# Performance work log

Hardware: AMD Instinct MI355X
Metric: run time of the kernel (lower is better)

## Reference

```python
import jax, jax.numpy as jnp
import numpy as np

BS, N = 8, 2000
ALPHA = 0.2  # LeakyReLU slope
NEG = -9e15


def _gat_head(x, adj, W, a):
    # x: [bs,N,Fin], W: [Fin,Fout], a: [2*Fout]
    h = x @ W                                   # [bs,N,F]
    F_ = W.shape[-1]
    # e_ij = lrelu(h_i . a[:F] + h_j . a[F:])  (decomposed form of concat+matmul)
    src = h @ a[:F_]                            # [bs,N]
    dst = h @ a[F_:]                            # [bs,N]
    e = jax.nn.leaky_relu(src[:, :, None] + dst[:, None, :], ALPHA)  # [bs,N,N]
    att = jnp.where(adj[None] > 0, e, NEG)
    att = jax.nn.softmax(att, axis=-1)
    return jax.nn.elu(att @ h)                  # [bs,N,F]


def _gat_multihead(x, adj, W, a):
    # W: [H,Fin,Fout], a: [H,2*Fout] -> concat heads on feature dim
    out = jax.vmap(_gat_head, in_axes=(None, None, 0, 0))(x, adj, W, a)  # [H,bs,N,F]
    H, bs, n, F_ = out.shape
    return jnp.moveaxis(out, 0, 2).reshape(bs, n, H * F_)


def setup_inputs() -> dict:
    key = jax.random.key(0)
    ks = jax.random.split(key, 20)
    g = 1.414

    def xavu(k, shape, gain=1.0):
        fan_in, fan_out = shape[-2], shape[-1]
        lim = gain * np.sqrt(6.0 / (fan_in + fan_out))
        return jax.random.uniform(k, shape, jnp.float32, -lim, lim)

    x = jax.random.normal(ks[0], (BS, N, 1), jnp.float32)
    adj = jax.random.randint(ks[1], (N, N), 0, 2).astype(jnp.float32)
    inp = {
        "x": x, "adj": adj,
        "W1": xavu(ks[2], (4, 1, 8), g), "a1": xavu(ks[3], (4, 16, 1), g)[..., 0],
        "W2": xavu(ks[4], (3, 32, 16), g), "a2": xavu(ks[5], (3, 32, 1), g)[..., 0],
        "pw1": xavu(ks[6], (32, 1))[:, 0], "pb1": jnp.zeros((1,), jnp.float32),
        "pw2": xavu(ks[7], (48, 1))[:, 0], "pb2": jnp.zeros((1,), jnp.float32),
        "fc1_w": xavu(ks[8], (3 * N, 600)), "fc1_b": jnp.zeros((600,), jnp.float32),
        "fc2_w": xavu(ks[9], (600, 256)), "fc2_b": jnp.zeros((256,), jnp.float32),
        "fc3_w": xavu(ks[10], (256, 64)), "fc3_b": jnp.zeros((64,), jnp.float32),
        "fc4_w": xavu(ks[11], (64, 32)), "fc4_b": jnp.zeros((32,), jnp.float32),
        "fc5_w": xavu(ks[12], (32, 2)), "fc5_b": jnp.zeros((2,), jnp.float32),
    }
    return inp


def reference(x, adj, W1, a1, W2, a2, pw1, pb1, pw2, pb2,
              fc1_w, fc1_b, fc2_w, fc2_b, fc3_w, fc3_b, fc4_w, fc4_b, fc5_w, fc5_b):
    # dropout layers are identity in eval mode
    x0 = jnp.mean(x, axis=-1)                       # [bs,N]
    h = _gat_multihead(x, adj, W1, a1)              # [bs,N,32]
    x1 = h @ pw1 + pb1                              # [bs,N]
    h = _gat_multihead(h, adj, W2, a2)              # [bs,N,48]
    x2 = h @ pw2 + pb2                              # [bs,N]
    z = jnp.concatenate([x0, x1, x2], axis=1)       # [bs,3N]
    z = jax.nn.elu(z @ fc1_w + fc1_b)
    z = jax.nn.elu(z @ fc2_w + fc2_b)
    z1 = jax.nn.elu(z @ fc3_w + fc3_b)              # output [bs,64]
    z = jax.nn.elu(z1 @ fc4_w + fc4_b)
    gat_out = z @ fc5_w + fc5_b                     # [bs,2]
    return (z1, gat_out)
```

## Files before the change

kernel.cpp:

```cpp
#include <hip/hip_runtime.h>
#include <hip/hip_bf16.h>
#include <cmath>

#define N_NODES 2000
#define BS 8

typedef __attribute__((ext_vector_type(8))) short short8v;
typedef __attribute__((ext_vector_type(4))) float float4v;

__device__ __forceinline__ float elu_f(float v) { return v > 0.f ? v : expm1f(v); }

__device__ __forceinline__ unsigned short f32_bf16u(float f) {
    __hip_bfloat16 h = __float2bfloat16(f);
    unsigned short u;
    __builtin_memcpy(&u, &h, 2);
    return u;
}
__device__ __forceinline__ short f32_bf16(float f) { return (short)f32_bf16u(f); }

__device__ __forceinline__ unsigned cvt_pk_bf16(float lo, float hi) {
    unsigned r;
    asm("v_cvt_pk_bf16_f32 %0, %1, %2" : "=v"(r) : "v"(lo), "v"(hi));
    return r;
}

__global__ __launch_bounds__(256) void pack_kernel(
    const float* __restrict__ adj, const float* __restrict__ x,
    const float* __restrict__ W1, const float* __restrict__ a1,
    unsigned* __restrict__ maskT32, short* __restrict__ hT,
    short* __restrict__ xb16,
    float* __restrict__ PQ1, float* __restrict__ md1) {
    __shared__ float2 redmm[256];
    int bx = blockIdx.x;
    int tid = threadIdx.x;
    if (bx < N_NODES) {
        int row = bx;
        int lane = tid & 63, wv = tid >> 6;
        for (int wq = wv; wq < 32; wq += 4) {
            int j = wq * 64 + lane;
            bool on = (j < N_NODES) && (adj[(size_t)row * N_NODES + j] > 0.f);
            unsigned long long bal = __ballot(on);
            if (lane == 0) {
                maskT32[(size_t)(2 * wq) * 2048 + row] = (unsigned)bal;
                maskT32[(size_t)(2 * wq + 1) * 2048 + row] = (unsigned)(bal >> 32);
            }
        }
        return;
    }
    if (bx == N_NODES) {
        for (int i = tid; i < 24 * 16 * 48; i += 256) {
            int bh = i / 768, rem = i % 768, f = rem / 48, n = N_NODES + rem % 48;
            hT[((size_t)bh * 16 + f) * 2048 + n] = 0;
        }
        return;
    }
    if (bx == N_NODES + 1) {
        for (int i = tid; i < BS * 2048; i += 256) {
            int b = i >> 11, n = i & 2047;
            xb16[i] = (n < N_NODES) ? f32_bf16(x[(size_t)b * N_NODES + n]) : 0;
        }
        return;
    }
    int bh = bx - (N_NODES + 2);
    int b = bh >> 2, h = bh & 3;
    float ws = 0.f, wd = 0.f;
    #pragma unroll
    for (int f = 0; f < 8; ++f) {
        float wv = W1[h * 8 + f];
        ws = fmaf(wv, a1[h * 16 + f], ws);
        wd = fmaf(wv, a1[h * 16 + 8 + f], wd);
    }
    float mn = 1e30f, mx = -1e30f;
    for (int n = tid; n < N_NODES; n += 256) {
        float v = x[(size_t)b * N_NODES + n];
        mn = fminf(mn, v); mx = fmaxf(mx, v);
    }
    redmm[tid] = make_float2(mn, mx);
    __syncthreads();
    for (int s = 128; s > 0; s >>= 1) {
        if (tid < s) {
            redmm[tid].x = fminf(redmm[tid].x, redmm[tid + s].x);
            redmm[tid].y = fmaxf(redmm[tid].y, redmm[tid + s].y);
        }
        __syncthreads();
    }
    float md = wd >= 0.f ? wd * redmm[0].y : wd * redmm[0].x;
    if (tid == 0) md1[bh] = md;
    float2* pq = (float2*)PQ1 + (size_t)bh * 2048;
    for (int n = tid; n < 2048; n += 256) {
        if (n < N_NODES) {
            float d = wd * x[(size_t)b * N_NODES + n] - md;
            pq[n] = make_float2(__expf(d), __expf(0.2f * d));
        } else {
            pq[n] = make_float2(0.f, 0.f);
        }
    }
}

__global__ __launch_bounds__(256) void att1_kernel(
    const unsigned* __restrict__ maskT32,
    const float* __restrict__ x, const short* __restrict__ xb16,
    const float* __restrict__ PQ1, const float* __restrict__ md1,
    const float* __restrict__ W1, const float* __restrict__ a1,
    float* __restrict__ pn1, float* __restrict__ pd1) {
    __shared__ float2 sPQ[1024];
    int tid = threadIdx.x;
    int head = blockIdx.y;
    int half = blockIdx.z & 1, b = blockIdx.z >> 1;
    int bh = b * 4 + head;
    int j0g = half * 1024;

    const float2* pq = (const float2*)PQ1 + (size_t)bh * 2048 + j0g;
    for (int i = tid; i < 1024; i += 256) sPQ[i] = pq[i];

    float ws = 0.f;
    #pragma unroll
    for (int f = 0; f < 8; ++f)
        ws = fmaf(W1[head * 8 + f], a1[head * 16 + f], ws);
    float md = md1[bh];
    __syncthreads();

    int lane = tid & 63;
    int wave = __builtin_amdgcn_readfirstlane(tid >> 6);
    int t = blockIdx.x * 4 + wave;
    if (t >= 125) return;
    int rs = lane & 15;
    int g = lane >> 4;
    int row = t * 16 + rs;

    float xr = x[(size_t)b * N_NODES + row];
    float u = ws * xr + md;
    float c = __expf(-0.8f * u);

    unsigned fill = (rs == 1) ? 0x3F803F80u : 0u;
    bool isx = (rs == 0);
    const short* xbp = xb16 + (size_t)b * 2048 + j0g;

    float4v acc = {0.f, 0.f, 0.f, 0.f};

    for (int jcl = 0; jcl < 32; ++jcl) {
        int jb = jcl * 32 + g * 8;
        float4 pqa0 = *(const float4*)(&sPQ[jb]);
        float4 pqa1 = *(const float4*)(&sPQ[jb + 2]);
        float4 pqa2 = *(const float4*)(&sPQ[jb + 4]);
        float4 pqa3 = *(const float4*)(&sPQ[jb + 6]);
        float w[8];
        w[0] = fmaxf(pqa0.x, c * pqa0.y); w[1] = fmaxf(pqa0.z, c * pqa0.w);
        w[2] = fmaxf(pqa1.x, c * pqa1.y); w[3] = fmaxf(pqa1.z, c * pqa1.w);
        w[4] = fmaxf(pqa2.x, c * pqa2.y); w[5] = fmaxf(pqa2.z, c * pqa2.w);
        w[6] = fmaxf(pqa3.x, c * pqa3.y); w[7] = fmaxf(pqa3.z, c * pqa3.w);
        unsigned mby = maskT32[(size_t)(half * 32 + jcl) * 2048 + row] >> (g * 8);
        #pragma unroll
        for (int e = 0; e < 8; ++e)
            w[e] = (mby & (1u << e)) ? w[e] : 0.f;
        uint4 au;
        au.x = cvt_pk_bf16(w[0], w[1]);
        au.y = cvt_pk_bf16(w[2], w[3]);
        au.z = cvt_pk_bf16(w[4], w[5]);
        au.w = cvt_pk_bf16(w[6], w[7]);
        short8v av;
        __builtin_memcpy(&av, &au, 16);
        uint4 bu;
        if (isx) bu = *(const uint4*)(xbp + jb);
        else bu = make_uint4(fill, fill, fill, fill);
        short8v bv;
        __builtin_memcpy(&bv, &bu, 16);
        acc = __builtin_amdgcn_mfma_f32_16x16x32_bf16(av, bv, acc, 0, 0, 0);
    }

    #pragma unroll
    for (int reg = 0; reg < 4; ++reg) {
        int crow = t * 16 + g * 4 + reg;
        if (rs == 0) pn1[(size_t)(half * 32 + bh) * N_NODES + crow] = acc[reg];
        if (rs == 1) pd1[(size_t)(half * 32 + bh) * N_NODES + crow] = acc[reg];
    }
}

__global__ __launch_bounds__(256) void finish1_kernel(
    const float* __restrict__ pn1, const float* __restrict__ pd1,
    const float* __restrict__ W1,
    float* __restrict__ o1) {
    int idx = blockIdx.x * 256 + threadIdx.x;
    if (idx >= BS * N_NODES) return;
    int b = idx / N_NODES, n = idx % N_NODES;
    #pragma unroll
    for (int head = 0; head < 4; ++head) {
        int bh = b * 4 + head;
        float num = pn1[(size_t)bh * N_NODES + n] + pn1[(size_t)(32 + bh) * N_NODES + n];
        float den = pd1[(size_t)bh * N_NODES + n] + pd1[(size_t)(32 + bh) * N_NODES + n];
        float ratio = den > 0.f ? num / den : 0.f;
        #pragma unroll
        for (int f = 0; f < 8; ++f) {
            float v = ratio * W1[head * 8 + f];
            o1[(size_t)idx * 32 + head * 8 + f] = v > 0.f ? v : expm1f(v);
        }
    }
}

__global__ __launch_bounds__(256) void prep2_kernel(
    const float* __restrict__ o1, const float* __restrict__ W2,
    const float* __restrict__ a2,
    short* __restrict__ hT, float* __restrict__ s2, float* __restrict__ d2) {
    __shared__ float sW[1536];
    int tid = threadIdx.x;
    for (int i = tid; i < 1536; i += 256) sW[i] = W2[i];
    __syncthreads();
    int idx = blockIdx.x * 256 + tid;
    if (idx >= BS * 3 * N_NODES) return;
    int b = idx / 6000, r = idx % 6000, h = r / N_NODES, n = r % N_NODES;
    int bh = b * 3 + h;
    float in[32];
    const float4* ip = (const float4*)(o1 + ((size_t)b * N_NODES + n) * 32);
    #pragma unroll
    for (int q = 0; q < 8; ++q) {
        float4 v = ip[q];
        in[4 * q] = v.x; in[4 * q + 1] = v.y; in[4 * q + 2] = v.z; in[4 * q + 3] = v.w;
    }
    float hv[16];
    #pragma unroll
    for (int f = 0; f < 16; ++f) hv[f] = 0.f;
    #pragma unroll
    for (int k = 0; k < 32; ++k) {
        float ik = in[k];
        #pragma unroll
        for (int f = 0; f < 16; ++f) hv[f] = fmaf(ik, sW[h * 512 + k * 16 + f], hv[f]);
    }
    float sr = 0.f, ds = 0.f;
    #pragma unroll
    for (int f = 0; f < 16; ++f) {
        hT[((size_t)bh * 16 + f) * 2048 + n] = f32_bf16(hv[f]);
        sr = fmaf(hv[f], a2[h * 32 + f], sr);
        ds = fmaf(hv[f], a2[h * 32 + 16 + f], ds);
    }
    s2[(size_t)bh * N_NODES + n] = sr;
    d2[(size_t)bh * N_NODES + n] = ds;
}

__global__ __launch_bounds__(256) void l2prep_kernel(
    const float* __restrict__ d2,
    float* __restrict__ PQ2, float* __restrict__ md2) {
    __shared__ float red[256];
    int bh = blockIdx.x;
    int tid = threadIdx.x;
    const float* dp = d2 + (size_t)bh * N_NODES;
    float mx = -1e30f;
    for (int n = tid; n < N_NODES; n += 256) mx = fmaxf(mx, dp[n]);
    red[tid] = mx;
    __syncthreads();
    for (int s = 128; s > 0; s >>= 1) {
        if (tid < s) red[tid] = fmaxf(red[tid], red[tid + s]);
        __syncthreads();
    }
    float md = red[0];
    if (tid == 0) md2[bh] = md;
    float2* pq = (float2*)PQ2 + (size_t)bh * 2048;
    for (int n = tid; n < 2048; n += 256) {
        if (n < N_NODES) {
            float d = dp[n] - md;
            pq[n] = make_float2(__expf(d), __expf(0.2f * d));
        } else {
            pq[n] = make_float2(0.f, 0.f);
        }
    }
}

__global__ __launch_bounds__(256) void att2_kernel(
    const unsigned* __restrict__ maskT32,
    const short* __restrict__ hT,
    const float* __restrict__ s2,
    const float* __restrict__ PQ2, const float* __restrict__ md2,
    float* __restrict__ pn2, float* __restrict__ pd2) {
    __shared__ float2 sPQ[1024];
    int tid = threadIdx.x;
    int head = blockIdx.y;
    int half = blockIdx.z & 1, b = blockIdx.z >> 1;
    int bh = b * 3 + head;
    int j0g = half * 1024;

    const float2* pq = (const float2*)PQ2 + (size_t)bh * 2048 + j0g;
    for (int i = tid; i < 1024; i += 256) sPQ[i] = pq[i];
    float md = md2[bh];
    __syncthreads();

    int lane = tid & 63;
    int wave = __builtin_amdgcn_readfirstlane(tid >> 6);
    int t = blockIdx.x * 4 + wave;
    if (t >= 125) return;
    int rs = lane & 15;
    int g = lane >> 4;
    int row = t * 16 + rs;

    float sv = s2[(size_t)bh * N_NODES + row];
    float u = sv + md;
    float c = __expf(-0.8f * u);
    const short* hb = hT + ((size_t)bh * 16 + rs) * 2048 + j0g;

    const unsigned one2 = 0x3F803F80u;
    uint4 ou = make_uint4(one2, one2, one2, one2);
    short8v onesv;
    __builtin_memcpy(&onesv, &ou, 16);

    float4v acc = {0.f, 0.f, 0.f, 0.f};
    float4v accd = {0.f, 0.f, 0.f, 0.f};

    for (int jcl = 0; jcl < 32; ++jcl) {
        int jb = jcl * 32 + g * 8;
        float4 pqa0 = *(const float4*)(&sPQ[jb]);
        float4 pqa1 = *(const float4*)(&sPQ[jb + 2]);
        float4 pqa2 = *(const float4*)(&sPQ[jb + 4]);
        float4 pqa3 = *(const float4*)(&sPQ[jb + 6]);
        float w[8];
        w[0] = fmaxf(pqa0.x, c * pqa0.y); w[1] = fmaxf(pqa0.z, c * pqa0.w);
        w[2] = fmaxf(pqa1.x, c * pqa1.y); w[3] = fmaxf(pqa1.z, c * pqa1.w);
        w[4] = fmaxf(pqa2.x, c * pqa2.y); w[5] = fmaxf(pqa2.z, c * pqa2.w);
        w[6] = fmaxf(pqa3.x, c * pqa3.y); w[7] = fmaxf(pqa3.z, c * pqa3.w);
        unsigned mby = maskT32[(size_t)(half * 32 + jcl) * 2048 + row] >> (g * 8);
        #pragma unroll
        for (int e = 0; e < 8; ++e)
            w[e] = (mby & (1u << e)) ? w[e] : 0.f;
        uint4 au;
        au.x = cvt_pk_bf16(w[0], w[1]);
        au.y = cvt_pk_bf16(w[2], w[3]);
        au.z = cvt_pk_bf16(w[4], w[5]);
        au.w = cvt_pk_bf16(w[6], w[7]);
        short8v av;
        __builtin_memcpy(&av, &au, 16);
        short8v bv = *(const short8v*)(hb + jb);
        acc = __builtin_amdgcn_mfma_f32_16x16x32_bf16(av, bv, acc, 0, 0, 0);
        accd = __builtin_amdgcn_mfma_f32_16x16x32_bf16(av, onesv, accd, 0, 0, 0);
    }

    #pragma unroll
    for (int reg = 0; reg < 4; ++reg) {
        int crow = t * 16 + g * 4 + reg;
        pn2[((size_t)(half * 24 + bh) * N_NODES + crow) * 16 + rs] = acc[reg];
        if (rs == 0) pd2[(size_t)(half * 24 + bh) * N_NODES + crow] = accd[reg];
    }
}

__global__ __launch_bounds__(256) void finish2_kernel(
    const float* __restrict__ pn2, const float* __restrict__ pd2,
    float* __restrict__ o2) {
    int idx = blockIdx.x * 256 + threadIdx.x;
    if (idx >= 24 * N_NODES) return;
    int bh = idx / N_NODES, n = idx % N_NODES;
    int b = bh / 3, h = bh % 3;
    float den = pd2[(size_t)bh * N_NODES + n] + pd2[(size_t)(24 + bh) * N_NODES + n];
    float inv = den > 0.f ? 1.0f / den : 0.f;
    const float4* pa = (const float4*)(pn2 + ((size_t)bh * N_NODES + n) * 16);
    const float4* pb = (const float4*)(pn2 + ((size_t)(24 + bh) * N_NODES + n) * 16);
    float* op = o2 + ((size_t)b * N_NODES + n) * 48 + h * 16;
    #pragma unroll
    for (int q = 0; q < 4; ++q) {
        float4 va = pa[q], vb = pb[q];
        float v0 = (va.x + vb.x) * inv;
        float v1 = (va.y + vb.y) * inv;
        float v2 = (va.z + vb.z) * inv;
        float v3 = (va.w + vb.w) * inv;
        op[4 * q + 0] = v0 > 0.f ? v0 : expm1f(v0);
        op[4 * q + 1] = v1 > 0.f ? v1 : expm1f(v1);
        op[4 * q + 2] = v2 > 0.f ? v2 : expm1f(v2);
        op[4 * q + 3] = v3 > 0.f ? v3 : expm1f(v3);
    }
}

__global__ __launch_bounds__(256) void fc1_splitk_kernel(
    const float* __restrict__ x,
    const float* __restrict__ o1, const float* __restrict__ o2,
    const float* __restrict__ pw1, const float* __restrict__ pb1,
    const float* __restrict__ pw2, const float* __restrict__ pb2,
    const float* __restrict__ W, float* __restrict__ partial) {
    const int K = 6000, O = 600, KS = 71;
    __shared__ float sz[BS][KS];
    int tid = threadIdx.x;
    int kt = blockIdx.y;
    int k0 = kt * KS;
    int len = (k0 + KS <= K) ? KS : (K - k0);
    float pb1v = pb1[0], pb2v = pb2[0];
    for (int i = tid; i < BS * len; i += 256) {
        int bb = i / len, k = k0 + i % len;
        float v;
        if (k < 2000) {
            v = x[bb * 2000 + k];
        } else if (k < 4000) {
            const float* op = o1 + ((size_t)bb * 2000 + (k - 2000)) * 32;
            float s = pb1v;
            #pragma unroll
            for (int q = 0; q < 32; ++q) s = fmaf(op[q], pw1[q], s);
            v = s;
        } else {
            const float* op = o2 + ((size_t)bb * 2000 + (k - 4000)) * 48;
            float s = pb2v;
            #pragma unroll
            for (int q = 0; q < 48; ++q) s = fmaf(op[q], pw2[q], s);
            v = s;
        }
        sz[bb][i % len] = v;
    }
    __syncthreads();
    int o = blockIdx.x * 256 + tid;
    float acc[BS] = {0.f, 0.f, 0.f, 0.f, 0.f, 0.f, 0.f, 0.f};
    if (o < O) {
        for (int k = 0; k < len; ++k) {
            float w = W[(size_t)(k0 + k) * O + o];
            #pragma unroll
            for (int b = 0; b < BS; ++b) acc[b] = fmaf(sz[b][k], w, acc[b]);
        }
        #pragma unroll
        for (int b = 0; b < BS; ++b)
            partial[((size_t)kt * BS + b) * O + o] = acc[b];
    }
}

__global__ __launch_bounds__(256) void fc2_splitk_kernel(
    const float* __restrict__ p1, const float* __restrict__ b1,
    const float* __restrict__ W, float* __restrict__ partial) {
    const int K = 600, O = 256, KS = 38;
    __shared__ float sz[BS][KS];
    int tid = threadIdx.x;
    int kt = blockIdx.y;
    int k0 = kt * KS;
    int k1 = k0 + KS < K ? k0 + KS : K;
    int len = k1 - k0;
    for (int i = tid; i < BS * len; i += 256) {
        int bb = i / len, k = k0 + i % len;
        float a = b1[k];
        #pragma unroll 5
        for (int q = 0; q < 85; ++q) a += p1[((size_t)q * BS + bb) * 600 + k];
        sz[bb][i % len] = elu_f(a);
    }
    __syncthreads();
    int o = tid;
    float acc[BS] = {0.f, 0.f, 0.f, 0.f, 0.f, 0.f, 0.f, 0.f};
    for (int k = 0; k < len; ++k) {
        float w = W[(size_t)(k0 + k) * O + o];
        #pragma unroll
        for (int b = 0; b < BS; ++b) acc[b] = fmaf(sz[b][k], w, acc[b]);
    }
    #pragma unroll
    for (int b = 0; b < BS; ++b)
        partial[((size_t)kt * BS + b) * O + o] = acc[b];
}

__global__ __launch_bounds__(256) void fc_tail_kernel(
    const float* __restrict__ p2, const float* __restrict__ b2,
    const float* __restrict__ w3, const float* __restrict__ b3,
    const float* __restrict__ w4, const float* __restrict__ b4,
    const float* __restrict__ w5, const float* __restrict__ b5,
    float* __restrict__ outp) {
    int b = blockIdx.x, tid = threadIdx.x;
    __shared__ float t2[256], red[256], z1[64], z4[32];
    {
        float a = b2[tid];
        #pragma unroll
        for (int kt = 0; kt < 16; ++kt) a += p2[((size_t)kt * BS + b) * 256 + tid];
        t2[tid] = elu_f(a);
    }
    __syncthreads();
    {
        int o = tid & 63, ks = tid >> 6;
        float a = 0.f;
        for (int k = ks; k < 256; k += 4) a = fmaf(t2[k], w3[k * 64 + o], a);
        red[tid] = a;
        __syncthreads();
        if (ks == 0) {
            float v = red[o] + red[64 + o] + red[128 + o] + red[192 + o] + b3[o];
            v = elu_f(v);
            z1[o] = v;
            outp[b * 64 + o] = v;
        }
    }
    __syncthreads();
    if (tid < 32) {
        float v = b4[tid];
        #pragma unroll
        for (int k = 0; k < 64; ++k) v = fmaf(z1[k], w4[k * 32 + tid], v);
        z4[tid] = elu_f(v);
    }
    __syncthreads();
    if (tid < 2) {
        float v = b5[tid];
        #pragma unroll
        for (int k = 0; k < 32; ++k) v = fmaf(z4[k], w5[k * 2 + tid], v);
        outp[BS * 64 + b * 2 + tid] = v;
    }
}

extern "C" void kernel_launch(void* const* d_in, const int* in_sizes, int n_in,
                              void* d_out, int out_size, void* d_ws, size_t ws_size,
                              hipStream_t stream) {
    const float* x    = (const float*)d_in[0];
    const float* adj  = (const float*)d_in[1];
    const float* W1   = (const float*)d_in[2];
    const float* a1   = (const float*)d_in[3];
    const float* W2   = (const float*)d_in[4];
    const float* a2   = (const float*)d_in[5];
    const float* pw1  = (const float*)d_in[6];
    const float* pb1  = (const float*)d_in[7];
    const float* pw2  = (const float*)d_in[8];
    const float* pb2  = (const float*)d_in[9];
    const float* fc1w = (const float*)d_in[10];
    const float* fc1b = (const float*)d_in[11];
    const float* fc2w = (const float*)d_in[12];
    const float* fc2b = (const float*)d_in[13];
    const float* fc3w = (const float*)d_in[14];
    const float* fc3b = (const float*)d_in[15];
    const float* fc4w = (const float*)d_in[16];
    const float* fc4b = (const float*)d_in[17];
    const float* fc5w = (const float*)d_in[18];
    const float* fc5b = (const float*)d_in[19];
    float* outp = (float*)d_out;

    float* ws = (float*)d_ws;
    size_t off = 0;
    auto alloc = [&](size_t n) {
        float* p = ws + off;
        off += (n + 63) & ~(size_t)63;
        return p;
    };
    float* o1   = alloc((size_t)BS * N_NODES * 32);
    float* s2   = alloc((size_t)24 * N_NODES);
    float* d2   = alloc((size_t)24 * N_NODES);
    short* hT   = (short*)alloc((size_t)24 * 16 * 2048 / 2);
    short* xb16 = (short*)alloc((size_t)BS * 2048 / 2);
    float* o2   = alloc((size_t)BS * N_NODES * 48);
    const int KT1 = 85;
    float* p1   = alloc((size_t)KT1 * BS * 600);
    float* p2   = alloc((size_t)16 * BS * 256);
    float* pn1  = alloc((size_t)2 * 32 * N_NODES);
    float* pd1  = alloc((size_t)2 * 32 * N_NODES);
    float* PQ1  = alloc((size_t)32 * 4096);
    float* md1  = alloc(64);
    float* pn2  = alloc((size_t)2 * 24 * N_NODES * 16);
    float* pd2  = alloc((size_t)2 * 24 * N_NODES);
    float* PQ2  = alloc((size_t)24 * 4096);
    float* md2  = alloc(64);
    unsigned* maskT32 = (unsigned*)alloc((size_t)64 * 2048);

    pack_kernel<<<N_NODES + 2 + 32, 256, 0, stream>>>(
        adj, x, W1, a1, maskT32, hT, xb16, PQ1, md1);
    att1_kernel<<<dim3(32, 4, BS * 2), 256, 0, stream>>>(
        maskT32, x, xb16, PQ1, md1, W1, a1, pn1, pd1);
    finish1_kernel<<<(BS * N_NODES + 255) / 256, 256, 0, stream>>>(pn1, pd1, W1, o1);
    prep2_kernel<<<(BS * 3 * N_NODES + 255) / 256, 256, 0, stream>>>(o1, W2, a2, hT, s2, d2);
    l2prep_kernel<<<24, 256, 0, stream>>>(d2, PQ2, md2);
    att2_kernel<<<dim3(32, 3, BS * 2), 256, 0, stream>>>(
        maskT32, hT, s2, PQ2, md2, pn2, pd2);
    finish2_kernel<<<(24 * N_NODES + 255) / 256, 256, 0, stream>>>(pn2, pd2, o2);
    fc1_splitk_kernel<<<dim3(3, KT1), 256, 0, stream>>>(
        x, o1, o2, pw1, pb1, pw2, pb2, fc1w, p1);
    fc2_splitk_kernel<<<dim3(1, 16), 256, 0, stream>>>(p1, fc1b, fc2w, p2);
    fc_tail_kernel<<<BS, 256, 0, stream>>>(
        p2, fc2b, fc3w, fc3b, fc4w, fc4b, fc5w, fc5b, outp);
}
```

Baseline: 156.5 us.

## Fuse finish1, prep2 and l2prep; compute layer-2 max via atomics and exp in att2

Merges the layer-1 finish kernel, the layer-2 projection kernel and the per-head max/exponent kernel into one kernel. The per-head max of d2 is reduced with wave shuffles plus an ordered-uint atomicMax, and att2 now computes the exp tables into shared memory itself. This removes two launches and the o1 reload and PQ2 round trip. In exchange each thread does three heads of projection, which raises register pressure and lowers thread count, and att2 recomputes exps redundantly per x-block.

```diff
diff --git a/kernel.cpp b/kernel.cpp
--- a/kernel.cpp
+++ b/kernel.cpp
@@ -24,12 +24,22 @@
     return r;
 }
 
+__device__ __forceinline__ unsigned f2ord(float f) {
+    unsigned b = __float_as_uint(f);
+    return (b & 0x80000000u) ? ~b : (b | 0x80000000u);
+}
+__device__ __forceinline__ float ord2f(unsigned u) {
+    unsigned b = (u & 0x80000000u) ? (u & 0x7FFFFFFFu) : ~u;
+    return __uint_as_float(b);
+}
+
 __global__ __launch_bounds__(256) void pack_kernel(
     const float* __restrict__ adj, const float* __restrict__ x,
     const float* __restrict__ W1, const float* __restrict__ a1,
     unsigned* __restrict__ maskT32, short* __restrict__ hT,
     short* __restrict__ xb16,
-    float* __restrict__ PQ1, float* __restrict__ md1) {
+    float* __restrict__ PQ1, float* __restrict__ md1,
+    unsigned* __restrict__ md2u) {
     __shared__ float2 redmm[256];
     int bx = blockIdx.x;
     int tid = threadIdx.x;
@@ -52,6 +62,7 @@
             int bh = i / 768, rem = i % 768, f = rem / 48, n = N_NODES + rem % 48;
             hT[((size_t)bh * 16 + f) * 2048 + n] = 0;
         }
+        if (tid < 24) md2u[tid] = 0u;
         return;
     }
     if (bx == N_NODES + 1) {
@@ -176,99 +187,89 @@
     }
 }
 
-__global__ __launch_bounds__(256) void finish1_kernel(
+__global__ __launch_bounds__(256) void prep2_kernel(
     const float* __restrict__ pn1, const float* __restrict__ pd1,
     const float* __restrict__ W1,
-    float* __restrict__ o1) {
-    int idx = blockIdx.x * 256 + threadIdx.x;
-    if (idx >= BS * N_NODES) return;
-    int b = idx / N_NODES, n = idx % N_NODES;
-    #pragma unroll
-    for (int head = 0; head < 4; ++head) {
-        int bh = b * 4 + head;
-        float num = pn1[(size_t)bh * N_NODES + n] + pn1[(size_t)(32 + bh) * N_NODES + n];
-        float den = pd1[(size_t)bh * N_NODES + n] + pd1[(size_t)(32 + bh) * N_NODES + n];
-        float ratio = den > 0.f ? num / den : 0.f;
-        #pragma unroll
-        for (int f = 0; f < 8; ++f) {
-            float v = ratio * W1[head * 8 + f];
-            o1[(size_t)idx * 32 + head * 8 + f] = v > 0.f ? v : expm1f(v);
-        }
-    }
-}
-
-__global__ __launch_bounds__(256) void prep2_kernel(
-    const float* __restrict__ o1, const float* __restrict__ W2,
-    const float* __restrict__ a2,
-    short* __restrict__ hT, float* __restrict__ s2, float* __restrict__ d2) {
+    const float* __restrict__ W2, const float* __restrict__ a2,
+    float* __restrict__ o1, short* __restrict__ hT,
+    float* __restrict__ s2, float* __restrict__ d2,
+    unsigned* __restrict__ md2u) {
     __shared__ float sW[1536];
     int tid = threadIdx.x;
     for (int i = tid; i < 1536; i += 256) sW[i] = W2[i];
     __syncthreads();
     int idx = blockIdx.x * 256 + tid;
-    if (idx >= BS * 3 * N_NODES) return;
-    int b = idx / 6000, r = idx % 6000, h = r / N_NODES, n = r % N_NODES;
-    int bh = b * 3 + h;
-    float in[32];
-    const float4* ip = (const float4*)(o1 + ((size_t)b * N_NODES + n) * 32);
-    #pragma unroll
-    for (int q = 0; q < 8; ++q) {
-        float4 v = ip[q];
-        in[4 * q] = v.x; in[4 * q + 1] = v.y; in[4 * q + 2] = v.z; in[4 * q + 3] = v.w;
-    }
-    float hv[16];
-    #pragma unroll
-    for (int f = 0; f < 16; ++f) hv[f] = 0.f;
-    #pragma unroll
-    for (int k = 0; k < 32; ++k) {
-        float ik = in[k];
-        #pragma unroll
-        for (int f = 0; f < 16; ++f) hv[f] = fmaf(ik, sW[h * 512 + k * 16 + f], hv[f]);
-    }
-    float sr = 0.f, ds = 0.f;
-    #pragma unroll
-    for (int f = 0; f < 16; ++f) {
-        hT[((size_t)bh * 16 + f) * 2048 + n] = f32_bf16(hv[f]);
-        sr = fmaf(hv[f], a2[h * 32 + f], sr);
-        ds = fmaf(hv[f], a2[h * 32 + 16 + f], ds);
-    }
-    s2[(size_t)bh * N_NODES + n] = sr;
-    d2[(size_t)bh * N_NODES + n] = ds;
-}
-
-__global__ __launch_bounds__(256) void l2prep_kernel(
-    const float* __restrict__ d2,
-    float* __restrict__ PQ2, float* __restrict__ md2) {
-    __shared__ float red[256];
-    int bh = blockIdx.x;
-    int tid = threadIdx.x;
-    const float* dp = d2 + (size_t)bh * N_NODES;
-    float mx = -1e30f;
-    for (int n = tid; n < N_NODES; n += 256) mx = fmaxf(mx, dp[n]);
-    red[tid] = mx;
-    __syncthreads();
-    for (int s = 128; s > 0; s >>= 1) {
-        if (tid < s) red[tid] = fmaxf(red[tid], red[tid + s]);
-        __syncthreads();
-    }
-    float md = red[0];
-    if (tid == 0) md2[bh] = md;
-    float2* pq = (float2*)PQ2 + (size_t)bh * 2048;
-    for (int n = tid; n < 2048; n += 256) {
-        if (n < N_NODES) {
-            float d = dp[n] - md;
-            pq[n] = make_float2(__expf(d), __expf(0.2f * d));
-        } else {
-            pq[n] = make_float2(0.f, 0.f);
-        }
+    bool act = idx < BS * N_NODES;
+    int b = act ? idx / N_NODES : 0;
+    int n = act ? idx % N_NODES : 0;
+
+    float o1f[32];
+    if (act) {
+        #pragma unroll
+        for (int head = 0; head < 4; ++head) {
+            int bh = b * 4 + head;
+            float num = pn1[(size_t)bh * N_NODES + n]
+                      + pn1[(size_t)(32 + bh) * N_NODES + n];
+            float den = pd1[(size_t)bh * N_NODES + n]
+                      + pd1[(size_t)(32 + bh) * N_NODES + n];
+            float ratio = den > 0.f ? num / den : 0.f;
+            #pragma unroll
+            for (int f = 0; f < 8; ++f) {
+                float v = ratio * W1[head * 8 + f];
+                o1f[head * 8 + f] = v > 0.f ? v : expm1f(v);
+            }
+        }
+        float4* op = (float4*)(o1 + (size_t)idx * 32);
+        #pragma unroll
+        for (int q = 0; q < 8; ++q)
+            op[q] = make_float4(o1f[4 * q], o1f[4 * q + 1], o1f[4 * q + 2], o1f[4 * q + 3]);
+    }
+
+    float dmax[3];
+    #pragma unroll
+    for (int h = 0; h < 3; ++h) {
+        dmax[h] = -1e30f;
+        if (act) {
+            int bh = b * 3 + h;
+            float hv[16];
+            #pragma unroll
+            for (int f = 0; f < 16; ++f) hv[f] = 0.f;
+            #pragma unroll
+            for (int k = 0; k < 32; ++k) {
+                float ik = o1f[k];
+                #pragma unroll
+                for (int f = 0; f < 16; ++f) hv[f] = fmaf(ik, sW[h * 512 + k * 16 + f], hv[f]);
+            }
+            float sr = 0.f, ds = 0.f;
+            #pragma unroll
+            for (int f = 0; f < 16; ++f) {
+                hT[((size_t)bh * 16 + f) * 2048 + n] = f32_bf16(hv[f]);
+                sr = fmaf(hv[f], a2[h * 32 + f], sr);
+                ds = fmaf(hv[f], a2[h * 32 + 16 + f], ds);
+            }
+            s2[(size_t)bh * N_NODES + n] = sr;
+            d2[(size_t)bh * N_NODES + n] = ds;
+            dmax[h] = ds;
+        }
+    }
+    int lane = tid & 63;
+    int b0 = __shfl(b, 0, 64);
+    #pragma unroll
+    for (int h = 0; h < 3; ++h) {
+        float m = (act && b == b0) ? dmax[h] : -1e30f;
+        #pragma unroll
+        for (int off = 32; off >= 1; off >>= 1)
+            m = fmaxf(m, __shfl_xor(m, off, 64));
+        if (lane == 0 && act) atomicMax(&md2u[b0 * 3 + h], f2ord(m));
+        if (act && b != b0) atomicMax(&md2u[b * 3 + h], f2ord(dmax[h]));
     }
 }
 
 __global__ __launch_bounds__(256) void att2_kernel(
     const unsigned* __restrict__ maskT32,
     const short* __restrict__ hT,
-    const float* __restrict__ s2,
-    const float* __restrict__ PQ2, const float* __restrict__ md2,
+    const float* __restrict__ s2, const float* __restrict__ d2,
+    const unsigned* __restrict__ md2u,
     float* __restrict__ pn2, float* __restrict__ pd2) {
     __shared__ float2 sPQ[1024];
     int tid = threadIdx.x;
@@ -277,9 +278,17 @@
     int bh = b * 3 + head;
     int j0g = half * 1024;
 
-    const float2* pq = (const float2*)PQ2 + (size_t)bh * 2048 + j0g;
-    for (int i = tid; i < 1024; i += 256) sPQ[i] = pq[i];
-    float md = md2[bh];
+    float md = ord2f(md2u[bh]);
+    const float* dp = d2 + (size_t)bh * N_NODES;
+    for (int i = tid; i < 1024; i += 256) {
+        int j = j0g + i;
+        if (j < N_NODES) {
+            float d = dp[j] - md;
+            sPQ[i] = make_float2(__expf(d), __expf(0.2f * d));
+        } else {
+            sPQ[i] = make_float2(0.f, 0.f);
+        }
+    }
     __syncthreads();
 
     int lane = tid & 63;
@@ -533,19 +542,17 @@
     float* md1  = alloc(64);
     float* pn2  = alloc((size_t)2 * 24 * N_NODES * 16);
     float* pd2  = alloc((size_t)2 * 24 * N_NODES);
-    float* PQ2  = alloc((size_t)24 * 4096);
-    float* md2  = alloc(64);
+    unsigned* md2u = (unsigned*)alloc(64);
     unsigned* maskT32 = (unsigned*)alloc((size_t)64 * 2048);
 
     pack_kernel<<<N_NODES + 2 + 32, 256, 0, stream>>>(
-        adj, x, W1, a1, maskT32, hT, xb16, PQ1, md1);
+        adj, x, W1, a1, maskT32, hT, xb16, PQ1, md1, md2u);
     att1_kernel<<<dim3(32, 4, BS * 2), 256, 0, stream>>>(
         maskT32, x, xb16, PQ1, md1, W1, a1, pn1, pd1);
-    finish1_kernel<<<(BS * N_NODES + 255) / 256, 256, 0, stream>>>(pn1, pd1, W1, o1);
-    prep2_kernel<<<(BS * 3 * N_NODES + 255) / 256, 256, 0, stream>>>(o1, W2, a2, hT, s2, d2);
-    l2prep_kernel<<<24, 256, 0, stream>>>(d2, PQ2, md2);
+    prep2_kernel<<<(BS * N_NODES + 255) / 256, 256, 0, stream>>>(
+        pn1, pd1, W1, W2, a2, o1, hT, s2, d2, md2u);
     att2_kernel<<<dim3(32, 3, BS * 2), 256, 0, stream>>>(
-        maskT32, hT, s2, PQ2, md2, pn2, pd2);
+        maskT32, hT, s2, d2, md2u, pn2, pd2);
     finish2_kernel<<<(24 * N_NODES + 255) / 256, 256, 0, stream>>>(pn2, pd2, o2);
     fc1_splitk_kernel<<<dim3(3, KT1), 256, 0, stream>>>(
         x, o1, o2, pw1, pb1, pw2, pb2, fc1w, p1);
```

Result: slower. 161.5 us (+3.2%).
